# Optimization experiments

Measured on AMD Instinct MI355X. Metric: run time of the kernel, lower is better.

Reference implementation:

```python
import jax, jax.numpy as jnp
import numpy as np

WS = 6      # window_size
SS = 3      # shift_size
NH = 8      # num_heads
DIM = 384
HD = DIM // NH
SCALE = HD ** -0.5


def _window_mask(H, W):
    # region ids: [:ss,:ss]=0, [:ss,ss:]=1, [ss:,:ss]=2, [ss:,ss:]=3
    row = (jnp.arange(H) >= SS).astype(jnp.int32)
    col = (jnp.arange(W) >= SS).astype(jnp.int32)
    region = row[:, None] * 2 + col[None, :]            # (H, W)
    region = jnp.roll(region, (-SS, -SS), axis=(0, 1))
    ids = region.reshape(H // WS, WS, W // WS, WS).transpose(0, 2, 1, 3)
    ids = ids.reshape(-1, WS * WS)                      # (nW, V)
    eq = ids[:, :, None] == ids[:, None, :]             # (nW, V, V)
    return jnp.where(eq, 0.0, -jnp.inf).astype(jnp.float32)


def setup_inputs():
    key = jax.random.key(0)
    k = jax.random.split(key, 5)
    B, H, W, D = 32, 48, 48, DIM
    return {
        "x": jax.random.normal(k[0], (B, H, W, D), jnp.float32),
        "w_qkv": jax.random.normal(k[1], (D, 3 * D), jnp.float32) * 0.02,
        "b_qkv": jax.random.normal(k[2], (3 * D,), jnp.float32) * 0.02,
        "w_proj": jax.random.normal(k[3], (D, D), jnp.float32) * 0.02,
        "b_proj": jax.random.normal(k[4], (D,), jnp.float32) * 0.02,
    }


def reference(x, w_qkv, b_qkv, w_proj, b_proj):
    B, H, W, D = x.shape
    nWh, nWw = H // WS, W // WS
    nW, V = nWh * nWw, WS * WS

    x = jnp.roll(x, (-SS, -SS), axis=(1, 2))
    amask = _window_mask(H, W)                          # (nW, V, V)

    # window partition -> (B*nW, V, D)
    xw = x.reshape(B, nWh, WS, nWw, WS, D).transpose(0, 1, 3, 2, 4, 5)
    xw = xw.reshape(B * nW, V, D)

    qkv = xw @ w_qkv + b_qkv                            # (M, V, 3D)
    qkv = qkv.reshape(B * nW, V, 3, NH, HD).transpose(2, 0, 3, 1, 4)
    q, k, v = qkv[0], qkv[1], qkv[2]                    # (M, NH, V, HD)

    scores = jnp.einsum("mhvd,mhud->mhvu", q, k) * SCALE
    scores = scores.reshape(B, nW, NH, V, V) + amask[None, :, None]
    attn = jax.nn.softmax(scores, axis=-1).reshape(B * nW, NH, V, V)

    out = jnp.einsum("mhvu,mhud->mhvd", attn, v)        # (M, NH, V, HD)
    out = out.transpose(0, 2, 1, 3).reshape(B * nW, V, D)

    # window reverse -> (B, H, W, D)
    out = out.reshape(B, nWh, nWw, WS, WS, D).transpose(0, 1, 3, 2, 4, 5)
    out = out.reshape(B, H, W, D)
    out = jnp.roll(out, (SS, SS), axis=(1, 2))
    return out @ w_proj + b_proj
```

## Files before the change

kernel.cpp:

```cpp
#include <hip/hip_runtime.h>
#include <hip/hip_bf16.h>

namespace {

constexpr int Bn   = 32;
constexpr int IMG  = 48;
constexpr int Dm   = 384;
constexpr int NHn  = 8;
constexpr int WSn  = 6;
constexpr int NWn  = 64;
constexpr int Mn   = Bn * NWn;
constexpr int Vn   = 36;
constexpr int ROWS = Mn * Vn;
constexpr int K3   = 3 * Dm;
constexpr int HEADS_E = Vn * 48;
constexpr float SCALE = 0.14433756729740643f;

using short8 = __attribute__((ext_vector_type(8))) short;
using f32x4  = __attribute__((ext_vector_type(4))) float;

__device__ __forceinline__ float bf2f(unsigned short u) {
    return __uint_as_float(((unsigned)u) << 16);
}
__device__ __forceinline__ unsigned short f2bf(float f) {
    unsigned u = __float_as_uint(f);
    u += 0x7FFFu + ((u >> 16) & 1u);
    return (unsigned short)(u >> 16);
}

__device__ __forceinline__ int invol(int f) {
    return (f & 56) | ((f ^ (f >> 3)) & 7);
}

__device__ __forceinline__ void gl_lds16(const unsigned short* g, unsigned short* l) {
    __builtin_amdgcn_global_load_lds(
        (const __attribute__((address_space(1))) unsigned int*)g,
        (__attribute__((address_space(3))) unsigned int*)l, 16, 0, 0);
}

__device__ __forceinline__ int gather_base(int row) {
    int m = row / Vn, v = row - m * Vn;
    int b = m >> 6, w = m & 63;
    int wh = w >> 3, ww = w & 7;
    int gh = wh * WSn + v / WSn;
    int gw = ww * WSn + v % WSn;
    int fi = (gh + 3) % IMG;
    int fj = (gw + 3) % IMG;
    return ((b * IMG + fi) * IMG + fj) * Dm;
}

__device__ __forceinline__ int region_id(int t, int wh, int ww) {
    int hi = (wh == 7) ? ((t / 6) < 3) : 1;
    int lo = (ww == 7) ? ((t % 6) < 3) : 1;
    return (hi << 1) | lo;
}

__global__ __launch_bounds__(256)
void gather_x(const float* __restrict__ x, unsigned short* __restrict__ xg)
{
    int idx = blockIdx.x * 256 + threadIdx.x;
    int row = idx / 96;
    int c4  = (idx - row * 96) * 4;
    float4 v = *(const float4*)(x + (size_t)gather_base(row) + c4);
    ushort4 o;
    o.x = f2bf(v.x); o.y = f2bf(v.y); o.z = f2bf(v.z); o.w = f2bf(v.w);
    *(ushort4*)(xg + (size_t)row * Dm + c4) = o;
}

__global__ __launch_bounds__(256)
void prep_w(const float* __restrict__ wq, const float* __restrict__ wp,
            unsigned short* __restrict__ wqT, unsigned short* __restrict__ wpT)
{
    int idx = blockIdx.x * 256 + threadIdx.x;
    if (idx < K3 * Dm) {
        int n = idx / Dm, k = idx - n * Dm;
        wqT[idx] = f2bf(wq[(size_t)k * K3 + n]);
    } else {
        int i2 = idx - K3 * Dm;
        if (i2 < Dm * Dm) {
            int n = i2 / Dm, k = i2 - n * Dm;
            wpT[i2] = f2bf(wp[(size_t)k * Dm + n]);
        }
    }
}

__global__ __launch_bounds__(256)
void qkv_mfma(const unsigned short* __restrict__ xg,
              const unsigned short* __restrict__ wqT,
              const float* __restrict__ bq,
              unsigned short* __restrict__ qh,
              unsigned short* __restrict__ kh,
              unsigned short* __restrict__ vh)
{
    __shared__ __align__(16) unsigned short As[3][128 * 32];
    __shared__ __align__(16) unsigned short Bs[3][128 * 32];

    const int tid  = threadIdx.x;
    const int wave = tid >> 6, lane = tid & 63;
    const int quad = lane >> 4, l15 = lane & 15;
    const int id = (blockIdx.x & 7) * 648 + (blockIdx.x >> 3);
    const int nT = id % (K3 / 128);
    const int mT = id / (K3 / 128);
    const int rowA0 = mT * 128, rowB0 = nT * 128;

    const int fS  = invol(lane);
    const int rS  = fS >> 2;
    const int kcS = (fS & 3) * 8;
    const unsigned short* gA = xg  + (size_t)(rowA0 + wave * 32 + rS) * Dm + kcS;
    const unsigned short* gB = wqT + (size_t)(rowB0 + wave * 32 + rS) * Dm + kcS;

    const int wm = wave >> 1, wn = wave & 1;
    int aoff[4], boff[4];
#pragma unroll
    for (int i = 0; i < 4; i++) {
        int R = wm * 64 + i * 16 + l15;
        aoff[i] = (R >> 4) * 512 + invol((R & 15) * 4 + quad) * 8;
        int S = wn * 64 + i * 16 + l15;
        boff[i] = (S >> 4) * 512 + invol((S & 15) * 4 + quad) * 8;
    }

    f32x4 acc[4][4];
#pragma unroll
    for (int i = 0; i < 4; i++)
#pragma unroll
        for (int j = 0; j < 4; j++) acc[i][j] = (f32x4){0.f, 0.f, 0.f, 0.f};

    auto STAGE = [&](int buf, int k0) {
        gl_lds16(gA + k0,           &As[buf][(wave * 32) * 32]);
        gl_lds16(gA + 16 * Dm + k0, &As[buf][(wave * 32 + 16) * 32]);
        gl_lds16(gB + k0,           &Bs[buf][(wave * 32) * 32]);
        gl_lds16(gB + 16 * Dm + k0, &Bs[buf][(wave * 32 + 16) * 32]);
    };
    auto COMPUTE = [&](int buf) {
        short8 af[4], bfr[4];
#pragma unroll
        for (int i = 0; i < 4; i++) af[i]  = *(const short8*)&As[buf][aoff[i]];
#pragma unroll
        for (int j = 0; j < 4; j++) bfr[j] = *(const short8*)&Bs[buf][boff[j]];
#pragma unroll
        for (int i = 0; i < 4; i++)
#pragma unroll
            for (int j = 0; j < 4; j++)
                acc[i][j] = __builtin_amdgcn_mfma_f32_16x16x32_bf16(af[i], bfr[j], acc[i][j], 0, 0, 0);
    };

    STAGE(0, 0);
    STAGE(1, 32);
#pragma unroll
    for (int t = 0; t < 10; ++t) {
        asm volatile("s_waitcnt vmcnt(4)" ::: "memory");
        __builtin_amdgcn_s_barrier();
        STAGE((t + 2) % 3, (t + 2) * 32);
        COMPUTE(t % 3);
    }
    asm volatile("s_waitcnt vmcnt(4)" ::: "memory");
    __builtin_amdgcn_s_barrier();
    COMPUTE(10 % 3);
    asm volatile("s_waitcnt vmcnt(0)" ::: "memory");
    __builtin_amdgcn_s_barrier();
    COMPUTE(11 % 3);

    unsigned short* outb = (nT < 3) ? qh : (nT < 6) ? kh : vh;
    const int csub = (nT < 3) ? 0 : (nT < 6) ? 384 : 768;
#pragma unroll
    for (int j = 0; j < 4; j++) {
        int col = rowB0 + wn * 64 + j * 16 + l15;
        float b = bq[col];
        int c  = col - csub;
        int hh = c / 48, dd = c - hh * 48;
#pragma unroll
        for (int i = 0; i < 4; i++) {
#pragma unroll
            for (int r = 0; r < 4; r++) {
                int row = rowA0 + wm * 64 + i * 16 + quad * 4 + r;
                int mm = row / 36, vv = row - mm * 36;
                outb[((size_t)(mm * 8 + hh) * 36 + vv) * 48 + dd] = f2bf(acc[i][j][r] + b);
            }
        }
    }
}

__global__ __launch_bounds__(256)
void attn_proj(const unsigned short* __restrict__ qh,
               const unsigned short* __restrict__ kh,
               const unsigned short* __restrict__ vh,
               const unsigned short* __restrict__ wpT,
               const float* __restrict__ bp,
               float* __restrict__ out)
{
    __shared__ __align__(16) unsigned short SMEM[23040];
    __shared__ int rowOut36[36];

    const int tid  = threadIdx.x;
    const int wave = tid >> 6, lane = tid & 63;
    const int quad = lane >> 4, l15 = lane & 15;
    const int m = blockIdx.x;
    const int w = m & 63, wh = w >> 3, ww = w & 7;
    const bool need_mask = (wh == 7) || (ww == 7);

    if (tid < 36) rowOut36[tid] = gather_base(m * 36 + tid);

    unsigned short* Plw = SMEM + wave * 2688;
    unsigned short* vws = SMEM + 10752 + wave * 3072;

    const short8 zf = {0, 0, 0, 0, 0, 0, 0, 0};

    {
        short8* vz = (short8*)(SMEM + 10752);
#pragma unroll
        for (int z = 0; z < 6; z++) vz[z * 256 + tid] = zf;
    }
    __syncthreads();

    f32x4 oacc2[2][3][3];

#pragma unroll
    for (int hi = 0; hi < 2; hi++) {
        const int h = wave * 2 + hi;
        const size_t hb = (size_t)(m * 8 + h) * HEADS_E;

        const unsigned short* qb = qh + hb;
        const unsigned short* kb = kh + hb;
        short8 qf[3][2], kf[3][2];
#pragma unroll
        for (int t = 0; t < 3; t++) {
            const unsigned short* qr = qb + (t * 16 + l15) * 48;
            qf[t][0] = *(const short8*)(qr + quad * 8);
            qf[t][1] = (quad < 2) ? *(const short8*)(qr + 32 + quad * 8) : zf;
            const unsigned short* kr = kb + (t * 16 + l15) * 48;
            kf[t][0] = *(const short8*)(kr + quad * 8);
            kf[t][1] = *(const short8*)(kr + 32 + quad * 8);
        }

        {
            const unsigned short* vb = vh + hb;
#pragma unroll
            for (int p = 0; p < 4; p++) {
                int c = p * 64 + lane;
                if (c < 216) {
                    short8 vv = *(const short8*)(vb + c * 8);
                    int v  = c / 6, d0 = (c - v * 6) * 8;
                    int g  = v >> 3, v7 = v & 7;
#pragma unroll
                    for (int jj = 0; jj < 8; jj++) {
                        int d = d0 + jj;
                        int slot = (g + (d & 7) + (d >> 3)) & 7;
                        vws[d * 64 + slot * 8 + v7] = (unsigned short)vv[jj];
                    }
                }
            }
        }

        f32x4 sacc[3][3];
#pragma unroll
        for (int i = 0; i < 3; i++)
#pragma unroll
            for (int j = 0; j < 3; j++) sacc[i][j] = (f32x4){0.f, 0.f, 0.f, 0.f};
        __builtin_amdgcn_s_setprio(1);
#pragma unroll
        for (int i = 0; i < 3; i++)
#pragma unroll
            for (int j = 0; j < 3; j++) {
                sacc[i][j] = __builtin_amdgcn_mfma_f32_16x16x32_bf16(qf[i][0], kf[j][0], sacc[i][j], 0, 0, 0);
                sacc[i][j] = __builtin_amdgcn_mfma_f32_16x16x32_bf16(qf[i][1], kf[j][1], sacc[i][j], 0, 0, 0);
            }
        __builtin_amdgcn_s_setprio(0);

#pragma unroll
        for (int i = 0; i < 3; i++) {
            float rs[4] = {0.f, 0.f, 0.f, 0.f};
            if (need_mask) {
#pragma unroll
                for (int j = 0; j < 3; j++) {
                    int C = j * 16 + l15;
                    int idc = region_id(C, wh, ww);
#pragma unroll
                    for (int r = 0; r < 4; r++) {
                        int R = i * 16 + quad * 4 + r;
                        int idr = region_id(R, wh, ww);
                        float s = sacc[i][j][r] * SCALE;
                        s = (C >= 36 || idr != idc) ? -1e30f : fminf(s, 30.f);
                        float e = __expf(s);
                        sacc[i][j][r] = e;
                        rs[r] += e;
                    }
                }
            } else {
#pragma unroll
                for (int j = 0; j < 3; j++) {
                    int C = j * 16 + l15;
#pragma unroll
                    for (int r = 0; r < 4; r++) {
                        float s = sacc[i][j][r] * SCALE;
                        s = (C >= 36) ? -1e30f : fminf(s, 30.f);
                        float e = __expf(s);
                        sacc[i][j][r] = e;
                        rs[r] += e;
                    }
                }
            }
#pragma unroll
            for (int r = 0; r < 4; r++) {
#pragma unroll
                for (int d = 1; d < 16; d <<= 1) rs[r] += __shfl_xor(rs[r], d, 16);
                rs[r] = 1.f / rs[r];
            }
#pragma unroll
            for (int j = 0; j < 3; j++)
#pragma unroll
                for (int r = 0; r < 4; r++) {
                    int R = i * 16 + quad * 4 + r;
                    int C = j * 16 + l15;
                    Plw[R * 56 + C] = f2bf(sacc[i][j][r] * rs[r]);
                }
        }
        __syncthreads();

        short8 pf[3][2], vf[3][2];
#pragma unroll
        for (int t = 0; t < 3; t++) {
            const unsigned short* pr = &Plw[(t * 16 + l15) * 56];
            pf[t][0] = *(const short8*)(pr + quad * 8);
            pf[t][1] = (quad < 2) ? *(const short8*)(pr + 32 + quad * 8) : zf;
            int d  = t * 16 + l15;
            int sb = (d & 7) + (d >> 3);
            vf[t][0] = *(const short8*)(vws + d * 64 + (((quad + sb) & 7) * 8));
            vf[t][1] = *(const short8*)(vws + d * 64 + (((quad + 4 + sb) & 7) * 8));
        }
#pragma unroll
        for (int i = 0; i < 3; i++)
#pragma unroll
            for (int j = 0; j < 3; j++) oacc2[hi][i][j] = (f32x4){0.f, 0.f, 0.f, 0.f};
        __builtin_amdgcn_s_setprio(1);
#pragma unroll
        for (int i = 0; i < 3; i++)
#pragma unroll
            for (int j = 0; j < 3; j++) {
                oacc2[hi][i][j] = __builtin_amdgcn_mfma_f32_16x16x32_bf16(pf[i][0], vf[j][0], oacc2[hi][i][j], 0, 0, 0);
                oacc2[hi][i][j] = __builtin_amdgcn_mfma_f32_16x16x32_bf16(pf[i][1], vf[j][1], oacc2[hi][i][j], 0, 0, 0);
            }
        __builtin_amdgcn_s_setprio(0);
    }

    __syncthreads();

#pragma unroll
    for (int hi = 0; hi < 2; hi++) {
        const int h = wave * 2 + hi;
#pragma unroll
        for (int i = 0; i < 3; i++)
#pragma unroll
            for (int r = 0; r < 4; r++) {
                int R = i * 16 + quad * 4 + r;
                if (R < 36) {
                    int band = R >> 4, f4 = (R & 15) * 4;
#pragma unroll
                    for (int j = 0; j < 3; j++) {
                        int k  = h * 48 + j * 16 + l15;
                        int ks = k >> 5, kk = k & 31;
                        SMEM[(ks * 3 + band) * 512 + invol(f4 + (kk >> 3)) * 8 + (kk & 7)]
                            = f2bf(oacc2[hi][i][j][r]);
                    }
                }
            }
    }
    __syncthreads();

    const int aoffP = invol(l15 * 4 + quad) * 8;
    const unsigned short* gBp = wpT + (size_t)(wave * 96 + l15) * 384 + quad * 8;
    f32x4 pacc[3][6];
#pragma unroll
    for (int i = 0; i < 3; i++)
#pragma unroll
        for (int j = 0; j < 6; j++) pacc[i][j] = (f32x4){0.f, 0.f, 0.f, 0.f};

#pragma unroll
    for (int ks = 0; ks < 12; ks++) {
        short8 bfr[6];
#pragma unroll
        for (int j = 0; j < 6; j++)
            bfr[j] = *(const short8*)(gBp + (size_t)j * 16 * 384 + ks * 32);
        short8 af[3];
#pragma unroll
        for (int i = 0; i < 3; i++)
            af[i] = *(const short8*)&SMEM[(ks * 3 + i) * 512 + aoffP];
#pragma unroll
        for (int i = 0; i < 3; i++)
#pragma unroll
            for (int j = 0; j < 6; j++)
                pacc[i][j] = __builtin_amdgcn_mfma_f32_16x16x32_bf16(af[i], bfr[j], pacc[i][j], 0, 0, 0);
    }

    float bpv[6];
#pragma unroll
    for (int j = 0; j < 6; j++) bpv[j] = bp[wave * 96 + j * 16 + l15];
#pragma unroll
    for (int i = 0; i < 3; i++)
#pragma unroll
        for (int r = 0; r < 4; r++) {
            int R = i * 16 + quad * 4 + r;
            if (R < 36) {
                float* orow = out + rowOut36[R];
#pragma unroll
                for (int j = 0; j < 6; j++)
                    orow[wave * 96 + j * 16 + l15] = pacc[i][j][r] + bpv[j];
            }
        }
}

}

extern "C" void kernel_launch(void* const* d_in, const int* in_sizes, int n_in,
                              void* d_out, int out_size, void* d_ws, size_t ws_size,
                              hipStream_t stream)
{
    const float* x  = (const float*)d_in[0];
    const float* wq = (const float*)d_in[1];
    const float* bq = (const float*)d_in[2];
    const float* wp = (const float*)d_in[3];
    const float* bp = (const float*)d_in[4];
    float* out = (float*)d_out;

    const size_t HE   = (size_t)Mn * NHn * HEADS_E;
    const size_t XG_E = (size_t)ROWS * Dm;
    unsigned short* qh  = (unsigned short*)d_ws;
    unsigned short* kh  = qh + HE;
    unsigned short* vh  = kh + HE;
    unsigned short* xg  = vh + HE;
    unsigned short* wqT = xg + XG_E;
    unsigned short* wpT = wqT + (size_t)K3 * Dm;

    prep_w   <<<(K3 * Dm + Dm * Dm + 255) / 256, 256, 0, stream>>>(wq, wp, wqT, wpT);
    gather_x <<<ROWS * (Dm / 4) / 256,            256, 0, stream>>>(x, xg);
    qkv_mfma <<<(ROWS / 128) * (K3 / 128),        256, 0, stream>>>(xg, wqT, bq, qh, kh, vh);
    attn_proj<<<Mn,                               256, 0, stream>>>(qh, kh, vh, wpT, bp, out);
}
```

Measured before the change: 442.5 us.

## Prefetch both heads' Q/K/V in attn_proj and drop intra-loop block barrier

Splits the per-head loop of attn_proj into load, softmax and PV stages. Q/K fragments for both heads are now loaded up front, and the second head's V global load is issued before the first head's PV, so memory latency overlaps with compute. The __syncthreads between the softmax writes and the PV reads is removed, which relies on Plw and vws being private to each wave. A __launch_bounds__ minimum of 3 blocks is also added, which caps registers while more fragments are live, so spills are a risk.

```diff
diff --git a/kernel.cpp b/kernel.cpp
--- a/kernel.cpp
+++ b/kernel.cpp
@@ -180,7 +180,7 @@
     }
 }
 
-__global__ __launch_bounds__(256)
+__global__ __launch_bounds__(256, 3)
 void attn_proj(const unsigned short* __restrict__ qh,
                const unsigned short* __restrict__ kh,
                const unsigned short* __restrict__ vh,
@@ -212,16 +212,12 @@
     }
     __syncthreads();
 
-    f32x4 oacc2[2][3][3];
-
-#pragma unroll
-    for (int hi = 0; hi < 2; hi++) {
-        const int h = wave * 2 + hi;
-        const size_t hb = (size_t)(m * 8 + h) * HEADS_E;
-
+    const size_t hb0 = (size_t)(m * 8 + wave * 2 + 0) * HEADS_E;
+    const size_t hb1 = (size_t)(m * 8 + wave * 2 + 1) * HEADS_E;
+
+    auto LOADQK = [&](size_t hb, short8 (*qf)[2], short8 (*kf)[2]) {
         const unsigned short* qb = qh + hb;
         const unsigned short* kb = kh + hb;
-        short8 qf[3][2], kf[3][2];
 #pragma unroll
         for (int t = 0; t < 3; t++) {
             const unsigned short* qr = qb + (t * 16 + l15) * 48;
@@ -231,26 +227,32 @@
             kf[t][0] = *(const short8*)(kr + quad * 8);
             kf[t][1] = *(const short8*)(kr + 32 + quad * 8);
         }
-
-        {
-            const unsigned short* vb = vh + hb;
-#pragma unroll
-            for (int p = 0; p < 4; p++) {
-                int c = p * 64 + lane;
-                if (c < 216) {
-                    short8 vv = *(const short8*)(vb + c * 8);
-                    int v  = c / 6, d0 = (c - v * 6) * 8;
-                    int g  = v >> 3, v7 = v & 7;
-#pragma unroll
-                    for (int jj = 0; jj < 8; jj++) {
-                        int d = d0 + jj;
-                        int slot = (g + (d & 7) + (d >> 3)) & 7;
-                        vws[d * 64 + slot * 8 + v7] = (unsigned short)vv[jj];
-                    }
+    };
+    auto LOADV = [&](size_t hb, short8* vvr) {
+        const unsigned short* vb = vh + hb;
+#pragma unroll
+        for (int p = 0; p < 4; p++) {
+            int c = p * 64 + lane;
+            if (c < 216) vvr[p] = *(const short8*)(vb + c * 8);
+        }
+    };
+    auto WRITEV = [&](const short8* vvr) {
+#pragma unroll
+        for (int p = 0; p < 4; p++) {
+            int c = p * 64 + lane;
+            if (c < 216) {
+                int v  = c / 6, d0 = (c - v * 6) * 8;
+                int g  = v >> 3, v7 = v & 7;
+#pragma unroll
+                for (int jj = 0; jj < 8; jj++) {
+                    int d = d0 + jj;
+                    int slot = (g + (d & 7) + (d >> 3)) & 7;
+                    vws[d * 64 + slot * 8 + v7] = (unsigned short)vvr[p][jj];
                 }
             }
         }
-
+    };
+    auto QKT_SM = [&](short8 (*qf)[2], short8 (*kf)[2]) {
         f32x4 sacc[3][3];
 #pragma unroll
         for (int i = 0; i < 3; i++)
@@ -265,7 +267,6 @@
                 sacc[i][j] = __builtin_amdgcn_mfma_f32_16x16x32_bf16(qf[i][1], kf[j][1], sacc[i][j], 0, 0, 0);
             }
         __builtin_amdgcn_s_setprio(0);
-
 #pragma unroll
         for (int i = 0; i < 3; i++) {
             float rs[4] = {0.f, 0.f, 0.f, 0.f};
@@ -314,8 +315,8 @@
                     Plw[R * 56 + C] = f2bf(sacc[i][j][r] * rs[r]);
                 }
         }
-        __syncthreads();
-
+    };
+    auto PV = [&](f32x4 (*oacc)[3]) {
         short8 pf[3][2], vf[3][2];
 #pragma unroll
         for (int t = 0; t < 3; t++) {
@@ -330,17 +331,32 @@
 #pragma unroll
         for (int i = 0; i < 3; i++)
 #pragma unroll
-            for (int j = 0; j < 3; j++) oacc2[hi][i][j] = (f32x4){0.f, 0.f, 0.f, 0.f};
+            for (int j = 0; j < 3; j++) oacc[i][j] = (f32x4){0.f, 0.f, 0.f, 0.f};
         __builtin_amdgcn_s_setprio(1);
 #pragma unroll
         for (int i = 0; i < 3; i++)
 #pragma unroll
             for (int j = 0; j < 3; j++) {
-                oacc2[hi][i][j] = __builtin_amdgcn_mfma_f32_16x16x32_bf16(pf[i][0], vf[j][0], oacc2[hi][i][j], 0, 0, 0);
-                oacc2[hi][i][j] = __builtin_amdgcn_mfma_f32_16x16x32_bf16(pf[i][1], vf[j][1], oacc2[hi][i][j], 0, 0, 0);
+                oacc[i][j] = __builtin_amdgcn_mfma_f32_16x16x32_bf16(pf[i][0], vf[j][0], oacc[i][j], 0, 0, 0);
+                oacc[i][j] = __builtin_amdgcn_mfma_f32_16x16x32_bf16(pf[i][1], vf[j][1], oacc[i][j], 0, 0, 0);
             }
         __builtin_amdgcn_s_setprio(0);
-    }
+    };
+
+    f32x4 oacc2[2][3][3];
+    short8 qf0[3][2], kf0[3][2], qf1[3][2], kf1[3][2];
+    short8 vv0[4], vv1[4];
+
+    LOADQK(hb0, qf0, kf0);
+    LOADQK(hb1, qf1, kf1);
+    LOADV(hb0, vv0);
+    WRITEV(vv0);
+    QKT_SM(qf0, kf0);
+    LOADV(hb1, vv1);
+    PV(oacc2[0]);
+    WRITEV(vv1);
+    QKT_SM(qf1, kf1);
+    PV(oacc2[1]);
 
     __syncthreads();
 
```

New measurement: 438.8 us. Within noise of the previous version (-0.8%).
